# Performance work log

Measured on AMD Instinct MI355X. Metric: run time of the kernel, lower is better.

The kernel has to match this reference:

```python
import jax, jax.numpy as jnp
import numpy as np

B, H, D = 4096, 1024, 4
SCALE = 20.0
EPS = 1e-7
LABEL_GATE = 0.01


def _layer_norm(x, g, b, eps=1e-5):
    mu = jnp.mean(x, axis=-1, keepdims=True)
    var = jnp.mean(jnp.square(x - mu), axis=-1, keepdims=True)
    return (x - mu) * jax.lax.rsqrt(var + eps) * g + b


def setup_inputs() -> dict:
    key = jax.random.key(0)
    ks = jax.random.split(key, 8)
    s = 0.02
    return {
        "pooled": jax.random.normal(ks[0], (B, H), dtype=jnp.float32),
        "labels": jax.random.uniform(ks[1], (B, D), dtype=jnp.float32),
        "ln1_g": jnp.ones((H,), jnp.float32),
        "ln1_b": jnp.zeros((H,), jnp.float32),
        "W1": jax.random.normal(ks[2], (H, H // 2), dtype=jnp.float32) * s,
        "b1": jnp.zeros((H // 2,), jnp.float32),
        "ln2_g": jnp.ones((H // 2,), jnp.float32),
        "ln2_b": jnp.zeros((H // 2,), jnp.float32),
        "W2": jax.random.normal(ks[3], (H // 2, H // 4), dtype=jnp.float32) * s,
        "b2": jnp.zeros((H // 4,), jnp.float32),
        "Wh": jax.random.normal(ks[4], (H // 4, D), dtype=jnp.float32) * s,
        "bh": jnp.zeros((D,), jnp.float32),
    }


def reference(pooled, labels, ln1_g, ln1_b, W1, b1, ln2_g, ln2_b, W2, b2, Wh, bh):
    # MLP head (dropout = identity in eval mode); exact GELU as in torch nn.GELU
    h1 = jax.nn.gelu(_layer_norm(pooled, ln1_g, ln1_b) @ W1 + b1, approximate=False)
    h2 = jax.nn.gelu(_layer_norm(h1, ln2_g, ln2_b) @ W2 + b2, approximate=False)
    logits = jax.nn.sigmoid(h2 @ Wh + bh)  # [B, D]

    # MSE term
    mse = jnp.mean(jnp.square(logits - labels))

    # Vectorized pairwise ordering loss over all i<j pairs and dims
    ldiff = labels[:, None, :] - labels[None, :, :]   # [B, B, D]
    pdiff = logits[:, None, :] - logits[None, :, :]   # [B, B, D]
    target_prob = jax.nn.sigmoid(SCALE * ldiff)
    pred_prob = jax.nn.sigmoid(SCALE * pdiff)
    bce = -target_prob * jnp.log(pred_prob + EPS) - (1.0 - target_prob) * jnp.log(1.0 - pred_prob + EPS)

    iu = jnp.triu(jnp.ones((B, B), dtype=bool), k=1)[:, :, None]  # i < j
    mask = iu & (jnp.abs(ldiff) > LABEL_GATE)
    cnt = jnp.sum(mask)
    ordering = jnp.where(cnt > 0, jnp.sum(jnp.where(mask, bce, 0.0)) / jnp.maximum(cnt, 1).astype(bce.dtype), 0.0)

    loss = 0.5 * mse + 0.5 * ordering
    return loss, logits
```

## Files before the change

kernel.cpp:

```cpp
#include <hip/hip_runtime.h>
#include <math.h>
#include <stdint.h>

typedef unsigned short u16;
typedef unsigned long long u64;
typedef __attribute__((ext_vector_type(8))) short bf16x8;
typedef __attribute__((ext_vector_type(4))) float f32x4;

#define RSQRT1_2F 0.70710678118654752440f

__device__ __forceinline__ u16 rne_bf16(float x) {
  unsigned u = __float_as_uint(x);
  return (u16)((u + 0x7FFFu + ((u >> 16) & 1u)) >> 16);
}
__device__ __forceinline__ float bf16_to_f(u16 h) {
  return __uint_as_float(((unsigned)h) << 16);
}
__device__ __forceinline__ void gload_lds16(const void* g, void* l) {
  __builtin_amdgcn_global_load_lds(
      (__attribute__((address_space(1))) void*)(uintptr_t)g,
      (__attribute__((address_space(3))) void*)(uintptr_t)l, 16, 0, 0);
}
__device__ __forceinline__ float rlane(float v, int sl) {
  return __uint_as_float((unsigned)__builtin_amdgcn_readlane((int)__float_as_uint(v), sl));
}
__device__ __forceinline__ float block_reduce_sum_f(float v, float* smem4) {
  #pragma unroll
  for (int off = 32; off > 0; off >>= 1) v += __shfl_down(v, off, 64);
  const int lane = threadIdx.x & 63;
  const int wid  = threadIdx.x >> 6;
  if (lane == 0) smem4[wid] = v;
  __syncthreads();
  float r = smem4[0] + smem4[1] + smem4[2] + smem4[3];
  __syncthreads();
  return r;
}
__device__ __forceinline__ float gelu_exact(float z) {
  return 0.5f * z * (1.0f + erff(z * RSQRT1_2F));
}

template<int H, int NPT>
__device__ __forceinline__ void ln_split_body(
    const float* __restrict__ x, const float* __restrict__ g,
    const float* __restrict__ b, u16* __restrict__ yhi, u16* __restrict__ ylo,
    int row, float* smem4) {
  const float* xr = x + (size_t)row * H;
  const int tid = threadIdx.x;
  float v[NPT];
  #pragma unroll
  for (int q = 0; q < NPT; ++q) v[q] = xr[tid + q * 256];
  float s = 0.f;
  #pragma unroll
  for (int q = 0; q < NPT; ++q) s += v[q];
  s = block_reduce_sum_f(s, smem4);
  const float mu = s * (1.0f / H);
  float s2 = 0.f;
  #pragma unroll
  for (int q = 0; q < NPT; ++q) { float d = v[q] - mu; s2 = fmaf(d, d, s2); }
  s2 = block_reduce_sum_f(s2, smem4);
  const float rstd = rsqrtf(s2 * (1.0f / H) + 1e-5f);
  #pragma unroll
  for (int q = 0; q < NPT; ++q) {
    const int c = tid + q * 256;
    const float y = (v[q] - mu) * rstd * g[c] + b[c];
    const u16 h = rne_bf16(y);
    const u16 lo = rne_bf16(y - bf16_to_f(h));
    yhi[(size_t)row * H + c] = h;
    ylo[(size_t)row * H + c] = lo;
  }
}

template<int K, int N>
__device__ __forceinline__ void wsplit_body(
    const float* __restrict__ W, u16* __restrict__ Whi, u16* __restrict__ Wlo,
    int ntile, int ktile, float* sm ) {
  const int t = threadIdx.x;
  const int n0 = ntile * 64, k0 = ktile * 64;
  #pragma unroll
  for (int q = 0; q < 16; ++q) {
    const int r = q * 4 + (t >> 6);
    sm[r * 65 + (t & 63)] = W[(size_t)(k0 + r) * N + n0 + (t & 63)];
  }
  __syncthreads();
  #pragma unroll
  for (int q = 0; q < 16; ++q) {
    const int nr = q * 4 + (t >> 6);
    const int kc = t & 63;
    const float v = sm[kc * 65 + nr];
    const u16 h = rne_bf16(v);
    const u16 lo = rne_bf16(v - bf16_to_f(h));
    Whi[(size_t)(n0 + nr) * K + k0 + kc] = h;
    Wlo[(size_t)(n0 + nr) * K + k0 + kc] = lo;
  }
}

__global__ __launch_bounds__(256) void prep_kernel(
    const float* __restrict__ pooled, const float* __restrict__ ln1_g,
    const float* __restrict__ ln1_b, const float* __restrict__ W1,
    const float* __restrict__ W2,
    u16* __restrict__ xhi, u16* __restrict__ xlo,
    u16* __restrict__ w1thi, u16* __restrict__ w1tlo,
    u16* __restrict__ w2thi, u16* __restrict__ w2tlo) {
  __shared__ float sm[64 * 65];
  const int bid = blockIdx.x;
  if (bid < 4096) {
    ln_split_body<1024, 4>(pooled, ln1_g, ln1_b, xhi, xlo, bid, sm);
  } else if (bid < 4224) {
    const int idx = bid - 4096;
    wsplit_body<1024, 512>(W1, w1thi, w1tlo, idx & 7, idx >> 3, sm);
  } else {
    const int idx = bid - 4224;
    wsplit_body<512, 256>(W2, w2thi, w2tlo, idx & 3, idx >> 2, sm);
  }
}

template<int BM, int NX, int MY, int K>
__global__ __launch_bounds__(256) void gemm_gelu_kernel(
    const u16* __restrict__ Ahi, const u16* __restrict__ Alo,
    const u16* __restrict__ Bhi, const u16* __restrict__ Blo,
    const float* __restrict__ bias, float* __restrict__ C, double* zclr) {
  constexpr int N  = NX * 64;
  constexpr int MF = BM / 32;
  constexpr int ABYTES = BM * 64;
  constexpr int AOFF = 2 * ABYTES;
  constexpr int BUF  = AOFF + 8192;
  constexpr int NS   = K / 32;
  __shared__ __align__(16) char sb[2 * BUF];

  if (zclr && blockIdx.x == 0 && threadIdx.x < 32) {
    zclr[threadIdx.x] = 0.0;
    zclr[32 + threadIdx.x] = 0.0;
    ((u64*)(zclr + 64))[threadIdx.x] = 0ull;
  }

  const int t = threadIdx.x, w = t >> 6, l = t & 63;
  const int lm = l & 15, lk = l >> 4;
  const int wm = w >> 1, wn = w & 1;
  int bid = (int)blockIdx.x;
  bid = (bid & 7) * ((NX * MY) >> 3) + (bid >> 3);
  const int my = bid / NX, nx = bid % NX;
  const int m0 = my * BM, n0 = nx * 64;

  f32x4 acc[MF][2];
  #pragma unroll
  for (int m = 0; m < MF; ++m)
    #pragma unroll
    for (int n = 0; n < 2; ++n)
      #pragma unroll
      for (int r = 0; r < 4; ++r) acc[m][n][r] = 0.f;

  auto STAGE = [&](int bufsel, int k0) {
    char* bb = sb + bufsel * BUF;
    if constexpr (BM == 64) {
      const int row = t >> 2, cq = (t & 3) * 16;
      const int col = cq ^ (((row >> 1) & 3) << 4);
      const size_t gb = ((size_t)(m0 + row) * K + k0) * 2 + col;
      gload_lds16((const char*)Ahi + gb, bb + t * 16);
      gload_lds16((const char*)Alo + gb, bb + ABYTES + t * 16);
    } else {
      const int half = t >> 7, tt = t & 127;
      const int row = tt >> 2, cq = (tt & 3) * 16;
      const int col = cq ^ (((row >> 1) & 3) << 4);
      const size_t gb = ((size_t)(m0 + row) * K + k0) * 2 + col;
      gload_lds16((const char*)(half ? Alo : Ahi) + gb,
                  bb + half * ABYTES + tt * 16);
    }
    {
      const int row = t >> 2, cq = (t & 3) * 16;
      const int col = cq ^ (((row >> 1) & 3) << 4);
      const size_t gb = ((size_t)(n0 + row) * K + k0) * 2 + col;
      gload_lds16((const char*)Bhi + gb, bb + AOFF + t * 16);
      gload_lds16((const char*)Blo + gb, bb + AOFF + 4096 + t * 16);
    }
  };
  auto COMPUTE = [&](int bufsel) {
    char* bb = sb + bufsel * BUF;
    bf16x8 ah[MF], al[MF], bhv[2], blv[2];
    #pragma unroll
    for (int m = 0; m < MF; ++m) {
      const int row = wm * (BM / 2) + m * 16 + lm;
      const int col = (lk * 16) ^ (((row >> 1) & 3) << 4);
      ah[m] = *(const bf16x8*)(bb + row * 64 + col);
      al[m] = *(const bf16x8*)(bb + ABYTES + row * 64 + col);
    }
    #pragma unroll
    for (int n = 0; n < 2; ++n) {
      const int row = wn * 32 + n * 16 + lm;
      const int col = (lk * 16) ^ (((row >> 1) & 3) << 4);
      bhv[n] = *(const bf16x8*)(bb + AOFF + row * 64 + col);
      blv[n] = *(const bf16x8*)(bb + AOFF + 4096 + row * 64 + col);
    }
    #pragma unroll
    for (int m = 0; m < MF; ++m)
      #pragma unroll
      for (int n = 0; n < 2; ++n) {
        acc[m][n] = __builtin_amdgcn_mfma_f32_16x16x32_bf16(ah[m], bhv[n], acc[m][n], 0, 0, 0);
        acc[m][n] = __builtin_amdgcn_mfma_f32_16x16x32_bf16(ah[m], blv[n], acc[m][n], 0, 0, 0);
        acc[m][n] = __builtin_amdgcn_mfma_f32_16x16x32_bf16(al[m], bhv[n], acc[m][n], 0, 0, 0);
      }
  };

  STAGE(0, 0);
  __syncthreads();
  for (int s = 0; s < NS; ++s) {
    if (s + 1 < NS) STAGE((s + 1) & 1, (s + 1) * 32);
    COMPUTE(s & 1);
    __syncthreads();
  }

  #pragma unroll
  for (int m = 0; m < MF; ++m)
    #pragma unroll
    for (int n = 0; n < 2; ++n) {
      const int col = n0 + wn * 32 + n * 16 + lm;
      const float bv = bias[col];
      #pragma unroll
      for (int r = 0; r < 4; ++r) {
        const int row = m0 + wm * (BM / 2) + m * 16 + lk * 4 + r;
        C[(size_t)row * N + col] = gelu_exact(acc[m][n][r] + bv);
      }
    }
}

template<int H, int NPT>
__global__ __launch_bounds__(256) void ln2_kernel(
    const float* __restrict__ x, const float* __restrict__ g,
    const float* __restrict__ b, u16* __restrict__ yhi, u16* __restrict__ ylo) {
  __shared__ float smem4[4];
  ln_split_body<H, NPT>(x, g, b, yhi, ylo, blockIdx.x, smem4);
}

__global__ __launch_bounds__(256) void head_kernel(
    const float* __restrict__ h2g, const float* __restrict__ Wh,
    const float* __restrict__ bh, const float* __restrict__ labels,
    float* __restrict__ logits_out, float* __restrict__ To,
    float* __restrict__ Eo, float* __restrict__ Lo,
    double* __restrict__ mse_slots) {
  const int lane = threadIdx.x & 63;
  const int wv   = threadIdx.x >> 6;
  const int row  = blockIdx.x * 4 + wv;
  const size_t base = (size_t)row * 256;
  float a0 = 0.f, a1 = 0.f, a2 = 0.f, a3 = 0.f;
  #pragma unroll
  for (int q = 0; q < 4; ++q) {
    const int k = lane + q * 64;
    const float hv = h2g[base + k];
    const float4 wv4 = *(const float4*)&Wh[k * 4];
    a0 = fmaf(hv, wv4.x, a0); a1 = fmaf(hv, wv4.y, a1);
    a2 = fmaf(hv, wv4.z, a2); a3 = fmaf(hv, wv4.w, a3);
  }
  #pragma unroll
  for (int off = 32; off > 0; off >>= 1) {
    a0 += __shfl_down(a0, off, 64);
    a1 += __shfl_down(a1, off, 64);
    a2 += __shfl_down(a2, off, 64);
    a3 += __shfl_down(a3, off, 64);
  }
  if (lane == 0) {
    const float z[4] = {a0 + bh[0], a1 + bh[1], a2 + bh[2], a3 + bh[3]};
    float msew = 0.f;
    #pragma unroll
    for (int d = 0; d < 4; ++d) {
      const float p = 1.0f / (1.0f + expf(-z[d]));
      const float lab = labels[row * 4 + d];
      logits_out[row * 4 + d] = p;
      To[row * 4 + d] = 20.0f * p;
      Eo[row * 4 + d] = expf(20.0f * p);
      Lo[row * 4 + d] = expf(20.0f * lab);
      const float df = p - lab;
      msew = fmaf(df, df, msew);
    }
    atomicAdd(&mse_slots[row & 31], (double)msew);
  }
}

#define GFUN(t) ((t) * 64 - (t) * ((t) - 1) / 2)
#define TGATE 0.0498339962f

__global__ __launch_bounds__(256) void pairwise_kernel(
    const float* __restrict__ To, const float* __restrict__ E,
    const float* __restrict__ L, double* __restrict__ slots) {
  const int lane = threadIdx.x & 63;
  const int wv   = threadIdx.x >> 6;
  const int idx  = blockIdx.x * 4 + wv;
  const int tile = idx >> 2;
  const int jbase = (idx & 3) * 16;

  int ti = (int)((129.0f - sqrtf(fmaxf(16641.0f - 8.0f * (float)tile, 0.f))) * 0.5f);
  if (ti < 0) ti = 0; if (ti > 63) ti = 63;
  while (ti > 0 && GFUN(ti) > tile) ti--;
  while (ti < 63 && GFUN(ti + 1) <= tile) ti++;
  const int tj = ti + (tile - GFUN(ti));
  const int i = ti * 64 + lane, j = tj * 64 + lane;

  const float4 e4 = *(const float4*)&E[(size_t)i * 4];
  const float4 t4 = *(const float4*)&To[(size_t)i * 4];
  const float4 l4 = *(const float4*)&L[(size_t)i * 4];
  const float Ei[4] = {e4.x, e4.y, e4.z, e4.w};
  const float Ti[4] = {t4.x, t4.y, t4.z, t4.w};
  const float Li[4] = {l4.x, l4.y, l4.z, l4.w};
  const float4 ej4 = *(const float4*)&E[(size_t)j * 4];
  const float4 tj4 = *(const float4*)&To[(size_t)j * 4];
  const float4 lj4 = *(const float4*)&L[(size_t)j * 4];
  const float Ejv[4] = {ej4.x, ej4.y, ej4.z, ej4.w};
  const float Tjv[4] = {tj4.x, tj4.y, tj4.z, tj4.w};
  const float Ljv[4] = {lj4.x, lj4.y, lj4.z, lj4.w};

  const bool diag = (ti == tj);
  float acc[4] = {0.f, 0.f, 0.f, 0.f};
  int cnt = 0;
  #pragma unroll
  for (int s = 0; s < 16; ++s) {
    const int jj = jbase + s;
    const bool jok = !diag || (jj > lane);
    #pragma unroll
    for (int d = 0; d < 4; ++d) {
      const float Ej = rlane(Ejv[d], jj);
      const float Tj = rlane(Tjv[d], jj);
      const float Lj = rlane(Ljv[d], jj);
      const float logse = __logf(Ei[d] + Ej);
      const float tt = Li[d] * __builtin_amdgcn_rcpf(Li[d] + Lj);
      const float bce = (logse - Tj) - tt * (Ti[d] - Tj);
      const bool m = jok && (fabsf(tt - 0.5f) > TGATE);
      acc[d] += m ? bce : 0.f;
      cnt += m ? 1 : 0;
    }
  }

  float tot = (acc[0] + acc[1]) + (acc[2] + acc[3]);
  #pragma unroll
  for (int off = 32; off > 0; off >>= 1) {
    tot += __shfl_down(tot, off, 64);
    cnt += __shfl_down(cnt, off, 64);
  }
  if (lane == 0) {
    const int sl = idx & 31;
    atomicAdd(&slots[32 + sl], (double)tot);
    atomicAdd((u64*)(slots + 64) + sl, (u64)cnt);
  }
}

__global__ void finalize_kernel(const double* __restrict__ slots,
                                float* __restrict__ out) {
  const int l = threadIdx.x;
  double m = (l < 32) ? slots[l] : 0.0;
  double o = (l < 32) ? slots[32 + l] : 0.0;
  double c = (l < 32) ? (double)((const u64*)(slots + 64))[l] : 0.0;
  #pragma unroll
  for (int off = 32; off > 0; off >>= 1) {
    m += __shfl_down(m, off, 64);
    o += __shfl_down(o, off, 64);
    c += __shfl_down(c, off, 64);
  }
  if (l == 0) {
    const double mse = m / (4096.0 * 4.0);
    const double ord = (c > 0.0) ? (o / c) : 0.0;
    out[0] = (float)(0.5 * mse + 0.5 * ord);
  }
}

extern "C" void kernel_launch(void* const* d_in, const int* in_sizes, int n_in,
                              void* d_out, int out_size, void* d_ws, size_t ws_size,
                              hipStream_t stream) {
  const float* pooled = (const float*)d_in[0];
  const float* labels = (const float*)d_in[1];
  const float* ln1_g  = (const float*)d_in[2];
  const float* ln1_b  = (const float*)d_in[3];
  const float* W1     = (const float*)d_in[4];
  const float* b1     = (const float*)d_in[5];
  const float* ln2_g  = (const float*)d_in[6];
  const float* ln2_b  = (const float*)d_in[7];
  const float* W2     = (const float*)d_in[8];
  const float* b2     = (const float*)d_in[9];
  const float* Wh     = (const float*)d_in[10];
  const float* bh     = (const float*)d_in[11];
  float* out = (float*)d_out;

  char* ws = (char*)d_ws;
  const size_t MB_ = 1048576;
  u16*   xhi   = (u16*)(ws + 0);
  u16*   xlo   = (u16*)(ws + 8 * MB_);
  u16*   w1thi = (u16*)(ws + 16 * MB_);
  u16*   w1tlo = (u16*)(ws + 17 * MB_);
  u16*   w2thi = (u16*)(ws + 18 * MB_);
  u16*   w2tlo = (u16*)(ws + 18 * MB_ + 262144);
  float* h1g   = (float*)(ws + 19 * MB_);
  u16*   h1nhi = (u16*)(ws + 27 * MB_);
  u16*   h1nlo = (u16*)(ws + 31 * MB_);
  float* h2g   = (float*)(ws + 35 * MB_);
  float* Eo    = (float*)(ws + 39 * MB_);
  float* To    = (float*)(ws + 39 * MB_ + 65536);
  float* Lo    = (float*)(ws + 39 * MB_ + 131072);
  double* slots = (double*)(ws + 39 * MB_ + 196608);

  prep_kernel<<<4256, 256, 0, stream>>>(pooled, ln1_g, ln1_b, W1, W2,
                                        xhi, xlo, w1thi, w1tlo, w2thi, w2tlo);
  gemm_gelu_kernel<64, 8, 64, 1024><<<512, 256, 0, stream>>>(
      xhi, xlo, w1thi, w1tlo, b1, h1g, nullptr);
  ln2_kernel<512, 2><<<4096, 256, 0, stream>>>(h1g, ln2_g, ln2_b, h1nhi, h1nlo);
  gemm_gelu_kernel<32, 4, 128, 512><<<512, 256, 0, stream>>>(
      h1nhi, h1nlo, w2thi, w2tlo, b2, h2g, slots);
  head_kernel<<<1024, 256, 0, stream>>>(
      h2g, Wh, bh, labels, out + 1, To, Eo, Lo, slots);
  pairwise_kernel<<<2080, 256, 0, stream>>>(To, Eo, Lo, slots);
  finalize_kernel<<<1, 64, 0, stream>>>(slots, out);
}
```

Measured before the change: 213.3 us.

## Rewrite pairwise BCE with stable softplus form and one wave per tile

The pairwise loss now passes raw scaled logits and labels, not precomputed exponentials. Each pair's BCE is computed as softplus(u) - sigmoid(v)*u, with the mask taken directly from the label difference. Each wave now covers a whole 64x64 tile with a templated diagonal/off-diagonal loop, the mask count uses a ballot popcount, and more reduction slots are used to spread atomic contention. This adds an extra exp per element in exchange for fewer loads, no per-element count accumulation, and fewer waves and atomics; it also removes overflow risk from exp(20x).

```diff
diff --git a/kernel.cpp b/kernel.cpp
--- a/kernel.cpp
+++ b/kernel.cpp
@@ -1,6 +1,7 @@
 #include <hip/hip_runtime.h>
 #include <math.h>
 #include <stdint.h>
+#include <type_traits>
 
 typedef unsigned short u16;
 typedef unsigned long long u64;
@@ -127,10 +128,10 @@
   constexpr int NS   = K / 32;
   __shared__ __align__(16) char sb[2 * BUF];
 
-  if (zclr && blockIdx.x == 0 && threadIdx.x < 32) {
-    zclr[threadIdx.x] = 0.0;
-    zclr[32 + threadIdx.x] = 0.0;
-    ((u64*)(zclr + 64))[threadIdx.x] = 0ull;
+  if (zclr && blockIdx.x == 0) {
+    const int t = threadIdx.x;
+    zclr[t] = 0.0; zclr[t + 256] = 0.0;
+    if (t < 32) zclr[t + 512] = 0.0;
   }
 
   const int t = threadIdx.x, w = t >> 6, l = t & 63;
@@ -234,8 +235,7 @@
     const float* __restrict__ h2g, const float* __restrict__ Wh,
     const float* __restrict__ bh, const float* __restrict__ labels,
     float* __restrict__ logits_out, float* __restrict__ To,
-    float* __restrict__ Eo, float* __restrict__ Lo,
-    double* __restrict__ mse_slots) {
+    float* __restrict__ Ao, double* __restrict__ mse_slots) {
   const int lane = threadIdx.x & 63;
   const int wv   = threadIdx.x >> 6;
   const int row  = blockIdx.x * 4 + wv;
@@ -265,8 +265,7 @@
       const float lab = labels[row * 4 + d];
       logits_out[row * 4 + d] = p;
       To[row * 4 + d] = 20.0f * p;
-      Eo[row * 4 + d] = expf(20.0f * p);
-      Lo[row * 4 + d] = expf(20.0f * lab);
+      Ao[row * 4 + d] = 20.0f * lab;
       const float df = p - lab;
       msew = fmaf(df, df, msew);
     }
@@ -275,16 +274,13 @@
 }
 
 #define GFUN(t) ((t) * 64 - (t) * ((t) - 1) / 2)
-#define TGATE 0.0498339962f
 
 __global__ __launch_bounds__(256) void pairwise_kernel(
-    const float* __restrict__ To, const float* __restrict__ E,
-    const float* __restrict__ L, double* __restrict__ slots) {
+    const float* __restrict__ To, const float* __restrict__ Ao,
+    double* __restrict__ slots) {
   const int lane = threadIdx.x & 63;
   const int wv   = threadIdx.x >> 6;
-  const int idx  = blockIdx.x * 4 + wv;
-  const int tile = idx >> 2;
-  const int jbase = (idx & 3) * 16;
+  const int tile = blockIdx.x * 4 + wv;
 
   int ti = (int)((129.0f - sqrtf(fmaxf(16641.0f - 8.0f * (float)tile, 0.f))) * 0.5f);
   if (ti < 0) ti = 0; if (ti > 63) ti = 63;
@@ -293,50 +289,48 @@
   const int tj = ti + (tile - GFUN(ti));
   const int i = ti * 64 + lane, j = tj * 64 + lane;
 
-  const float4 e4 = *(const float4*)&E[(size_t)i * 4];
   const float4 t4 = *(const float4*)&To[(size_t)i * 4];
-  const float4 l4 = *(const float4*)&L[(size_t)i * 4];
-  const float Ei[4] = {e4.x, e4.y, e4.z, e4.w};
+  const float4 a4 = *(const float4*)&Ao[(size_t)i * 4];
   const float Ti[4] = {t4.x, t4.y, t4.z, t4.w};
-  const float Li[4] = {l4.x, l4.y, l4.z, l4.w};
-  const float4 ej4 = *(const float4*)&E[(size_t)j * 4];
+  const float Ai[4] = {a4.x, a4.y, a4.z, a4.w};
   const float4 tj4 = *(const float4*)&To[(size_t)j * 4];
-  const float4 lj4 = *(const float4*)&L[(size_t)j * 4];
-  const float Ejv[4] = {ej4.x, ej4.y, ej4.z, ej4.w};
+  const float4 aj4 = *(const float4*)&Ao[(size_t)j * 4];
   const float Tjv[4] = {tj4.x, tj4.y, tj4.z, tj4.w};
-  const float Ljv[4] = {lj4.x, lj4.y, lj4.z, lj4.w};
-
-  const bool diag = (ti == tj);
+  const float Ajv[4] = {aj4.x, aj4.y, aj4.z, aj4.w};
+
   float acc[4] = {0.f, 0.f, 0.f, 0.f};
-  int cnt = 0;
-  #pragma unroll
-  for (int s = 0; s < 16; ++s) {
-    const int jj = jbase + s;
-    const bool jok = !diag || (jj > lane);
-    #pragma unroll
-    for (int d = 0; d < 4; ++d) {
-      const float Ej = rlane(Ejv[d], jj);
-      const float Tj = rlane(Tjv[d], jj);
-      const float Lj = rlane(Ljv[d], jj);
-      const float logse = __logf(Ei[d] + Ej);
-      const float tt = Li[d] * __builtin_amdgcn_rcpf(Li[d] + Lj);
-      const float bce = (logse - Tj) - tt * (Ti[d] - Tj);
-      const bool m = jok && (fabsf(tt - 0.5f) > TGATE);
-      acc[d] += m ? bce : 0.f;
-      cnt += m ? 1 : 0;
-    }
-  }
+  u64 cnt = 0;
+
+  auto body = [&](auto diagc) {
+    constexpr bool DIAG = decltype(diagc)::value;
+    #pragma unroll 8
+    for (int s = 0; s < 64; ++s) {
+      #pragma unroll
+      for (int d = 0; d < 4; ++d) {
+        const float Tj = rlane(Tjv[d], s);
+        const float Aj = rlane(Ajv[d], s);
+        const float u = Ti[d] - Tj;
+        const float v = Ai[d] - Aj;
+        const float sp = fmaxf(u, 0.f) + __logf(1.f + __expf(-fabsf(u)));
+        const float sg = __builtin_amdgcn_rcpf(1.f + __expf(-v));
+        const float bce = sp - sg * u;
+        bool m = fabsf(v) > 0.2f;
+        if constexpr (DIAG) m = m && (s > lane);
+        acc[d] += m ? bce : 0.f;
+        cnt += (u64)__popcll(__ballot(m));
+      }
+    }
+  };
+  if (ti == tj) body(std::integral_constant<bool, true>{});
+  else          body(std::integral_constant<bool, false>{});
 
   float tot = (acc[0] + acc[1]) + (acc[2] + acc[3]);
   #pragma unroll
-  for (int off = 32; off > 0; off >>= 1) {
-    tot += __shfl_down(tot, off, 64);
-    cnt += __shfl_down(cnt, off, 64);
-  }
+  for (int off = 32; off > 0; off >>= 1) tot += __shfl_down(tot, off, 64);
   if (lane == 0) {
-    const int sl = idx & 31;
+    const int sl = tile & 255;
     atomicAdd(&slots[32 + sl], (double)tot);
-    atomicAdd((u64*)(slots + 64) + sl, (u64)cnt);
+    atomicAdd((u64*)(slots + 288) + sl, cnt);
   }
 }
 
@@ -344,8 +338,12 @@
                                 float* __restrict__ out) {
   const int l = threadIdx.x;
   double m = (l < 32) ? slots[l] : 0.0;
-  double o = (l < 32) ? slots[32 + l] : 0.0;
-  double c = (l < 32) ? (double)((const u64*)(slots + 64))[l] : 0.0;
+  double o = 0.0, c = 0.0;
+  #pragma unroll
+  for (int k = 0; k < 4; ++k) {
+    o += slots[32 + l + k * 64];
+    c += (double)((const u64*)(slots + 288))[l + k * 64];
+  }
   #pragma unroll
   for (int off = 32; off > 0; off >>= 1) {
     m += __shfl_down(m, off, 64);
@@ -388,9 +386,8 @@
   u16*   h1nhi = (u16*)(ws + 27 * MB_);
   u16*   h1nlo = (u16*)(ws + 31 * MB_);
   float* h2g   = (float*)(ws + 35 * MB_);
-  float* Eo    = (float*)(ws + 39 * MB_);
-  float* To    = (float*)(ws + 39 * MB_ + 65536);
-  float* Lo    = (float*)(ws + 39 * MB_ + 131072);
+  float* To    = (float*)(ws + 39 * MB_);
+  float* Ao    = (float*)(ws + 39 * MB_ + 65536);
   double* slots = (double*)(ws + 39 * MB_ + 196608);
 
   prep_kernel<<<4256, 256, 0, stream>>>(pooled, ln1_g, ln1_b, W1, W2,
@@ -401,7 +398,7 @@
   gemm_gelu_kernel<32, 4, 128, 512><<<512, 256, 0, stream>>>(
       h1nhi, h1nlo, w2thi, w2tlo, b2, h2g, slots);
   head_kernel<<<1024, 256, 0, stream>>>(
-      h2g, Wh, bh, labels, out + 1, To, Eo, Lo, slots);
-  pairwise_kernel<<<2080, 256, 0, stream>>>(To, Eo, Lo, slots);
+      h2g, Wh, bh, labels, out + 1, To, Ao, slots);
+  pairwise_kernel<<<520, 256, 0, stream>>>(To, Ao, slots);
   finalize_kernel<<<1, 64, 0, stream>>>(slots, out);
 }
```

Result: faster. 203.5 us (-4.6%).
